# Kernel tuning notes

Measured on AMD Instinct MI355X. Metric: run time of the kernel, lower is better.

## Reference

```python
import jax, jax.numpy as jnp
import numpy as np

B, C, H, W = 32, 384, 32, 32
NH = 4            # num_heads
CC = 192          # conv_channels = ceil(384/2)
HID = 1536        # mlp hidden = 4*dim
EPS = 1e-6


def _ln2d(x, w, b):
    # LayerNorm over channel axis of NCHW
    u = x.mean(1, keepdims=True)
    s = ((x - u) ** 2).mean(1, keepdims=True)
    return w[:, None, None] * ((x - u) * jax.lax.rsqrt(s + EPS)) + b[:, None, None]


def setup_inputs() -> dict:
    key = jax.random.key(0)
    ks = jax.random.split(key, 8)
    f = lambda k, shp, sc: jax.random.normal(k, shp, jnp.float32) * sc
    return {
        "x": f(ks[0], (B, C, H, W), 1.0),
        "conv_w": f(ks[1], (CC, 1, 3, 3), 0.1),
        "conv_b": jnp.zeros((CC,), jnp.float32),
        "nxca_w": jnp.ones((C,), jnp.float32),
        "nxca_b": jnp.zeros((C,), jnp.float32),
        "temp": jnp.ones((NH, 1, 1), jnp.float32),
        "qkv_w": f(ks[2], (3 * C, C), 0.05),
        "qkv_b": jnp.zeros((3 * C,), jnp.float32),
        "proj_w": f(ks[3], (C, C), 0.05),
        "proj_b": jnp.zeros((C,), jnp.float32),
        "norm_w": jnp.ones((C,), jnp.float32),
        "norm_b": jnp.zeros((C,), jnp.float32),
        "fc1_w": f(ks[4], (HID, C), 0.05),
        "fc1_b": jnp.zeros((HID,), jnp.float32),
        "fc2_w": f(ks[5], (C, HID), 0.05),
        "fc2_b": jnp.zeros((C,), jnp.float32),
        "gamma_xca": jnp.ones((C,), jnp.float32),
        "gamma": jnp.ones((C,), jnp.float32),
    }


def reference(x, conv_w, conv_b, nxca_w, nxca_b, temp, qkv_w, qkv_b,
              proj_w, proj_b, norm_w, norm_b, fc1_w, fc1_b, fc2_w, fc2_b,
              gamma_xca, gamma):
    b, c, h, w = x.shape
    n = h * w
    hd = c // NH
    # depthwise 3x3 conv on first CC channels (in-place in torch -> shortcut
    # taken AFTER the conv, faithfully reproduced here)
    xc = jax.lax.conv_general_dilated(
        x[:, :CC], conv_w, (1, 1), ((1, 1), (1, 1)), feature_group_count=CC
    ) + conv_b[None, :, None, None]
    x = jnp.concatenate([xc, x[:, CC:]], axis=1)
    shortcut = x
    # XCA branch
    y = _ln2d(x, nxca_w, nxca_b)
    yf = y.reshape(b, c, n).transpose(0, 2, 1)                       # [B,N,C]
    qkv = (yf @ qkv_w.T + qkv_b).reshape(b, n, 3, NH, hd).transpose(2, 0, 3, 1, 4)
    q, k, v = qkv[0], qkv[1], qkv[2]                                  # [B,h,N,hd]
    q = q / jnp.maximum(jnp.linalg.norm(q, axis=-1, keepdims=True), 1e-12)
    k = k / jnp.maximum(jnp.linalg.norm(k, axis=-1, keepdims=True), 1e-12)
    attn = jax.nn.softmax(jnp.einsum('bhnd,bhmd->bhnm', q, k) * temp, axis=-1)
    o = jnp.einsum('bhnm,bhmd->bhnd', attn, v).transpose(0, 2, 1, 3).reshape(b, n, c)
    o = (o @ proj_w.T + proj_b).transpose(0, 2, 1).reshape(b, c, h, w)
    x = shortcut + gamma_xca[None, :, None, None] * o
    # MLP branch
    shortcut2 = x
    z = _ln2d(x, norm_w, norm_b).transpose(0, 2, 3, 1).reshape(b, n, c)
    z = jax.nn.gelu(z @ fc1_w.T + fc1_b, approximate=False) @ fc2_w.T + fc2_b
    z = z.reshape(b, h, w, c).transpose(0, 3, 1, 2)
    return shortcut2 + gamma[None, :, None, None] * z
```

## Files before the change

### kernel.cpp

```cpp
#include <hip/hip_runtime.h>
#include <cstdint>

typedef unsigned short u16;
typedef unsigned int u32;
typedef unsigned long long u64;
typedef __attribute__((ext_vector_type(4))) float f32x4;
typedef __attribute__((ext_vector_type(8))) __bf16 bf16x8;
typedef __attribute__((ext_vector_type(8))) u16 u16x8;

#define DEV __device__ __forceinline__

DEV u16 cvt16(float f) {
  __bf16 h = (__bf16)f;
  return __builtin_bit_cast(u16, h);
}
DEV u16 f2bf(float f) {
  u32 u = __builtin_bit_cast(u32, f);
  u += 0x7fffu + ((u >> 16) & 1u);
  return (u16)(u >> 16);
}
DEV float bflo2f(u32 packed) { return __builtin_bit_cast(float, packed << 16); }
DEV float bfhi2f(u32 packed) { return __builtin_bit_cast(float, packed & 0xffff0000u); }

DEV void g2l16(void* lds_wave_base, const void* gsrc) {
  __builtin_amdgcn_global_load_lds(
      (const __attribute__((address_space(1))) u32*)gsrc,
      (__attribute__((address_space(3))) u32*)lds_wave_base, 16, 0, 0);
}

DEV float gelu_tanh(float v) {
  float z = v * (0.7978845608f + 0.0356774081f * v * v);
  float e = __expf(2.0f * z);
  float th = 1.0f - 2.0f / (e + 1.0f);
  return 0.5f * v * (1.0f + th);
}

__global__ __launch_bounds__(256) void conv_k(const float* __restrict__ x,
                                              const float* __restrict__ cw,
                                              const float* __restrict__ cb,
                                              float* __restrict__ xc) {
  const int bc = blockIdx.x;
  const int c = bc % 384;
  const int p4 = threadIdx.x * 4;
  const float* xp = x + ((size_t)bc << 10);
  float* op = xc + ((size_t)bc << 10) + p4;
  if (c >= 192) {
    *(f32x4*)op = *(const f32x4*)(xp + p4);
    return;
  }
  const int hh = p4 >> 5, ww0 = p4 & 31;
  const float* wb = cw + c * 9;
  float b0 = cb[c];
  float a0 = b0, a1 = b0, a2 = b0, a3 = b0;
#pragma unroll
  for (int dy = 0; dy < 3; ++dy) {
    int y = hh + dy - 1;
    if ((unsigned)y < 32u) {
      const float* rp = xp + y * 32 + ww0;
      f32x4 m = *(const f32x4*)rp;
      float lft = (ww0 > 0) ? rp[-1] : 0.f;
      float rgt = (ww0 < 28) ? rp[4] : 0.f;
      float w0 = wb[dy * 3], w1 = wb[dy * 3 + 1], w2 = wb[dy * 3 + 2];
      a0 += lft * w0 + m[0] * w1 + m[1] * w2;
      a1 += m[0] * w0 + m[1] * w1 + m[2] * w2;
      a2 += m[1] * w0 + m[2] * w1 + m[3] * w2;
      a3 += m[2] * w0 + m[3] * w1 + rgt * w2;
    }
  }
  f32x4 r = {a0, a1, a2, a3};
  *(f32x4*)op = r;
}

__global__ __launch_bounds__(256) void cvt4_k(const float* __restrict__ s0,
                                              const float* __restrict__ s1,
                                              const float* __restrict__ s2,
                                              const float* __restrict__ s3,
                                              u16* __restrict__ d0,
                                              u16* __restrict__ d1,
                                              u16* __restrict__ d2,
                                              u16* __restrict__ d3) {
  int id = blockIdx.x * 256 + threadIdx.x;
  if (id < 442368) d0[id] = f2bf(s0[id]);
  else if (id < 589824) d1[id - 442368] = f2bf(s1[id - 442368]);
  else if (id < 1179648) d2[id - 589824] = f2bf(s2[id - 589824]);
  else if (id < 1769472) d3[id - 1179648] = f2bf(s3[id - 1179648]);
}

__global__ __launch_bounds__(256) void ln_t_k(const float* __restrict__ X,
                                              const float* __restrict__ w,
                                              const float* __restrict__ bsh,
                                              u16* __restrict__ Y) {
  __shared__ float tile[384][33];
  __shared__ float ps[8][32], ps2[8][32];
  __shared__ float mean_s[32], rstd_s[32];
  const int b = blockIdx.y;
  const int p0 = blockIdx.x * 32;
  const int t = threadIdx.x;
  const int pl = t & 31, cg = t >> 5;
  const float* xb = X + (((size_t)b * 384) << 10) + p0 + pl;
  float s = 0.f, s2 = 0.f;
  for (int c = cg; c < 384; c += 8) {
    float v = xb[(size_t)c << 10];
    tile[c][pl] = v;
    s += v;
    s2 += v * v;
  }
  ps[cg][pl] = s;
  ps2[cg][pl] = s2;
  __syncthreads();
  if (t < 32) {
    float a = 0.f, a2 = 0.f;
#pragma unroll
    for (int g = 0; g < 8; ++g) { a += ps[g][t]; a2 += ps2[g][t]; }
    float mu = a * (1.f / 384.f);
    float var = a2 * (1.f / 384.f) - mu * mu;
    mean_s[t] = mu;
    rstd_s[t] = rsqrtf(var + 1e-6f);
  }
  __syncthreads();
  const int cl = t & 63, pg = t >> 6;
  for (int p = pg; p < 32; p += 4) {
    float mu = mean_s[p], rs = rstd_s[p];
    size_t orow = (((size_t)b << 10) + p0 + p) * 384;
#pragma unroll
    for (int cc = 0; cc < 6; ++cc) {
      int c = cc * 64 + cl;
      float v = (tile[c][p] - mu) * rs * w[c] + bsh[c];
      Y[orow + c] = f2bf(v);
    }
  }
}

__global__ __launch_bounds__(256) void normqk_k(u16* __restrict__ QKV,
                                                const float* __restrict__ temp) {
  const int t = threadIdx.x;
  const int w = t >> 6, l = t & 63;
  const int rg = l >> 4, li = l & 15;
  const int tok = blockIdx.x * 16 + w * 4 + rg;
  u16* rowp = QKV + (size_t)tok * 1152;
#pragma unroll
  for (int seg = 0; seg < 8; ++seg) {
    const int h = seg & 3, isK = seg >> 2;
    u16* p = rowp + isK * 384 + h * 96 + li * 6;
    u32 a = *(const u32*)p;
    u32 b2 = *(const u32*)(p + 2);
    u32 c = *(const u32*)(p + 4);
    float v[6] = {bflo2f(a), bfhi2f(a), bflo2f(b2), bfhi2f(b2), bflo2f(c), bfhi2f(c)};
    float ss = 0.f;
#pragma unroll
    for (int i = 0; i < 6; ++i) ss += v[i] * v[i];
#pragma unroll
    for (int mk = 1; mk < 16; mk <<= 1) ss += __shfl_xor(ss, mk, 64);
    float sc = 1.0f / fmaxf(sqrtf(ss), 1e-12f);
    if (!isK) sc *= temp[h];
    u32 o0 = (u32)f2bf(v[0] * sc) | ((u32)f2bf(v[1] * sc) << 16);
    u32 o1 = (u32)f2bf(v[2] * sc) | ((u32)f2bf(v[3] * sc) << 16);
    u32 o2 = (u32)f2bf(v[4] * sc) | ((u32)f2bf(v[5] * sc) << 16);
    *(u32*)p = o0;
    *(u32*)(p + 2) = o1;
    *(u32*)(p + 4) = o2;
  }
}

__global__ __launch_bounds__(256) void attn_k(const u16* __restrict__ QKV,
                                              const u16* __restrict__ Vg,
                                              u16* __restrict__ O,
                                              const float* __restrict__ temp) {
  __shared__ u16 Kt[2][8192];
  __shared__ u16 Vt[2][6144];
  __shared__ u16 Pt[4][2304];
  const int t = threadIdx.x;
  const int w = t >> 6, l = t & 63;
  const int l15 = l & 15, kg = l >> 4;
  const int id = blockIdx.x;
  const int xcd = id & 7, jj = id >> 3;
  const int bh = xcd * 16 + (jj >> 3);
  const int qb = jj & 7;
  const int b = bh >> 2, h = bh & 3;
  const int q0 = qb * 128 + w * 32;
  const u16* Qb = QKV + (size_t)b * 1024 * 1152;
  const char* Kbg = (const char*)QKV + (size_t)b * 1024 * 2304 + 768 + 192 * h;
  const u16* Vbg = Vg + (size_t)bh * 98304;
  const float T = fabsf(temp[h]);

  u32 sK[4], sV[3];
#pragma unroll
  for (int j = 0; j < 4; ++j) {
    u32 s = w * 4096 + j * 1024 + l * 16;
    u32 row = s >> 8, rem = s & 255;
    u32 X = rem ^ ((row & 7) << 4);
    sK[j] = (X < 192) ? (row * 2304 + X) : 0u;
  }
#pragma unroll
  for (int j = 0; j < 3; ++j) {
    u32 s = w * 3072 + j * 1024 + l * 16;
    u32 u = s ^ (((s >> 7) & 7) << 4);
    sV[j] = (u >> 7) * 2048 + (u & 127);
  }
  u32 cs[3];
#pragma unroll
  for (int kk = 0; kk < 3; ++kk)
    cs[kk] = (u32)((kk * 64 + kg * 16) ^ ((l15 & 7) << 4));

  bf16x8 qf[2][3];
#pragma unroll
  for (int f = 0; f < 2; ++f) {
    const u16* qp = Qb + (size_t)(q0 + f * 16 + l15) * 1152 + h * 96 + kg * 8;
#pragma unroll
    for (int kk = 0; kk < 3; ++kk) qf[f][kk] = *(const bf16x8*)(qp + kk * 32);
  }
  f32x4 oa[2][6];
#pragma unroll
  for (int f = 0; f < 2; ++f)
#pragma unroll
    for (int d = 0; d < 6; ++d) oa[f][d] = {0.f, 0.f, 0.f, 0.f};
  float l_r[2][4] = {{0.f, 0.f, 0.f, 0.f}, {0.f, 0.f, 0.f, 0.f}};
  __bf16* Pw = (__bf16*)&Pt[w][0];

#define STAGE(buf, kv0)                                                        \
  {                                                                            \
    const char* kb = Kbg + (size_t)(kv0) * 2304;                               \
    const char* vb = (const char*)Vbg + (size_t)(kv0) * 2;                     \
    char* kd = (char*)&Kt[buf][0] + w * 4096;                                  \
    char* vd = (char*)&Vt[buf][0] + w * 3072;                                  \
    g2l16(kd, kb + sK[0]);                                                     \
    g2l16(kd + 1024, kb + sK[1]);                                              \
    g2l16(kd + 2048, kb + sK[2]);                                              \
    g2l16(kd + 3072, kb + sK[3]);                                              \
    g2l16(vd, vb + sV[0]);                                                     \
    g2l16(vd + 1024, vb + sV[1]);                                              \
    g2l16(vd + 2048, vb + sV[2]);                                              \
  }

  STAGE(0, 0);
  for (int tt = 0; tt < 16; ++tt) {
    const int cur = tt & 1;
    if (tt < 15) {
      STAGE(cur ^ 1, (tt + 1) * 64);
      asm volatile("s_waitcnt vmcnt(7)" ::: "memory");
    } else {
      asm volatile("s_waitcnt vmcnt(0)" ::: "memory");
    }
    __builtin_amdgcn_s_barrier();
    const char* Kc = (const char*)&Kt[cur][0];
    const char* Vc = (const char*)&Vt[cur][0];
    f32x4 s0[4], s1[4];
#pragma unroll
    for (int n = 0; n < 4; ++n) { s0[n] = {0.f, 0.f, 0.f, 0.f}; s1[n] = {0.f, 0.f, 0.f, 0.f}; }
#pragma unroll
    for (int n = 0; n < 4; ++n) {
      const char* krow = Kc + ((n * 16 + l15) << 8);
#pragma unroll
      for (int kk = 0; kk < 3; ++kk) {
        bf16x8 kf = *(const bf16x8*)(krow + cs[kk]);
        s0[n] = __builtin_amdgcn_mfma_f32_16x16x32_bf16(qf[0][kk], kf, s0[n], 0, 0, 0);
        s1[n] = __builtin_amdgcn_mfma_f32_16x16x32_bf16(qf[1][kk], kf, s1[n], 0, 0, 0);
      }
    }
#pragma unroll
    for (int n = 0; n < 4; ++n) {
#pragma unroll
      for (int j = 0; j < 4; ++j) {
        float p0 = __expf(s0[n][j] - T);
        float p1 = __expf(s1[n][j] - T);
        l_r[0][j] += p0;
        l_r[1][j] += p1;
        Pw[(kg * 4 + j) * 72 + n * 16 + l15] = (__bf16)p0;
        Pw[(16 + kg * 4 + j) * 72 + n * 16 + l15] = (__bf16)p1;
      }
    }
#pragma unroll
    for (int kk = 0; kk < 2; ++kk) {
      bf16x8 pf0 = *(const bf16x8*)(Pw + (size_t)l15 * 72 + kk * 32 + kg * 8);
      bf16x8 pf1 = *(const bf16x8*)(Pw + (size_t)(16 + l15) * 72 + kk * 32 + kg * 8);
#pragma unroll
      for (int d = 0; d < 6; ++d) {
        bf16x8 vf = *(const bf16x8*)(Vc + ((d * 16 + l15) << 7) + cs[kk]);
        oa[0][d] = __builtin_amdgcn_mfma_f32_16x16x32_bf16(pf0, vf, oa[0][d], 0, 0, 0);
        oa[1][d] = __builtin_amdgcn_mfma_f32_16x16x32_bf16(pf1, vf, oa[1][d], 0, 0, 0);
      }
    }
    __builtin_amdgcn_s_barrier();
  }
#undef STAGE
  float inv[2][4];
#pragma unroll
  for (int f = 0; f < 2; ++f)
#pragma unroll
    for (int j = 0; j < 4; ++j) {
      float sum = l_r[f][j];
#pragma unroll
      for (int mk = 1; mk < 16; mk <<= 1) sum += __shfl_xor(sum, mk, 64);
      inv[f][j] = 1.0f / sum;
    }
#pragma unroll
  for (int f = 0; f < 2; ++f)
#pragma unroll
    for (int d = 0; d < 6; ++d)
#pragma unroll
      for (int j = 0; j < 4; ++j) {
        int tok = q0 + f * 16 + kg * 4 + j;
        O[((size_t)b * 1024 + tok) * 384 + h * 96 + d * 16 + l15] =
            f2bf(oa[f][d][j] * inv[f][j]);
      }
}

template <int EPI, int SWZ>
__global__ __launch_bounds__(256) void gemm_k(const u16* __restrict__ A,
                                              const u16* __restrict__ B, int M,
                                              int N, int K,
                                              const float* __restrict__ bias,
                                              const float* gamma,
                                              const float* res, void* outp,
                                              int nbx) {
  __shared__ u16 SM[16384];
  const int t = threadIdx.x;
  const int w = t >> 6, l = t & 63;
  const int l15 = l & 15, kg = l >> 4;
  int bx, by;
  if (SWZ == 1) {
    int id = blockIdx.x;
    int xcd = id & 7, jj = id >> 3;
    int q = jj / nbx;
    bx = jj - q * nbx;
    by = xcd * 32 + q;
  } else if (SWZ == 2) {
    int id = blockIdx.x;
    int xcd = id & 7, jj = id >> 3;
    by = jj % 3;
    bx = (jj / 3) * 8 + xcd;
  } else {
    bx = blockIdx.x; by = blockIdx.y;
  }
  const int m0 = by * 128, n0 = bx * 128;
  const int wr = w >> 1, wc = w & 1;

  const int off1 = w * 1024 + l * 16;
  const int off2 = 4096 + w * 1024 + l * 16;
  const int r1 = off1 >> 6, c1 = off1 & 63;
  const int r2 = off2 >> 6, c2 = off2 & 63;
  const size_t ldab = (size_t)K * 2;
  const char* pa1 = (const char*)A + (size_t)(m0 + r1) * ldab + c1;
  const char* pa2 = (const char*)A + (size_t)(m0 + r2) * ldab + c2;
  const char* pb1 = (const char*)B + (size_t)(n0 + r1) * ldab + c1;
  const char* pb2 = (const char*)B + (size_t)(n0 + r2) * ldab + c2;
  char* SMc = (char*)SM;

  f32x4 acc[4][4];
#pragma unroll
  for (int m = 0; m < 4; ++m)
#pragma unroll
    for (int n = 0; n < 4; ++n) acc[m][n] = {0.f, 0.f, 0.f, 0.f};

  const int nkt = K >> 5;
  {
    char* ad = SMc + w * 1024;
    char* bd = SMc + 16384 + w * 1024;
    g2l16(ad, pa1); g2l16(ad + 4096, pa2);
    g2l16(bd, pb1); g2l16(bd + 4096, pb2);
  }
  for (int kt = 0; kt < nkt; ++kt) {
    const int buf = kt & 1;
    if (kt + 1 < nkt) {
      const size_t o = (size_t)(kt + 1) * 64;
      char* ad = SMc + (buf ^ 1) * 8192 + w * 1024;
      char* bd = SMc + 16384 + (buf ^ 1) * 8192 + w * 1024;
      g2l16(ad, pa1 + o); g2l16(ad + 4096, pa2 + o);
      g2l16(bd, pb1 + o); g2l16(bd + 4096, pb2 + o);
      asm volatile("s_waitcnt vmcnt(4)" ::: "memory");
    } else {
      asm volatile("s_waitcnt vmcnt(0)" ::: "memory");
    }
    __builtin_amdgcn_s_barrier();
    __builtin_amdgcn_sched_barrier(0);
    const u16* Ab = SM + buf * 4096;
    const u16* Bb = SM + 8192 + buf * 4096;
    bf16x8 af[4], bfr[4];
#pragma unroll
    for (int m = 0; m < 4; ++m)
      af[m] = *(const bf16x8*)(Ab + (wr * 64 + m * 16 + l15) * 32 + kg * 8);
#pragma unroll
    for (int n = 0; n < 4; ++n)
      bfr[n] = *(const bf16x8*)(Bb + (wc * 64 + n * 16 + l15) * 32 + kg * 8);
#pragma unroll
    for (int m = 0; m < 4; ++m)
#pragma unroll
      for (int n = 0; n < 4; ++n)
        acc[m][n] = __builtin_amdgcn_mfma_f32_16x16x32_bf16(af[m], bfr[n], acc[m][n], 0, 0, 0);
    __builtin_amdgcn_sched_barrier(0);
    __builtin_amdgcn_s_barrier();
  }

  if (EPI == 2) {
    float* out = (float*)outp;
#pragma unroll
    for (int m = 0; m < 4; ++m) {
#pragma unroll
      for (int n = 0; n < 4; ++n) {
        int tok = n0 + wc * 64 + n * 16 + l15;
        int bb = tok >> 10, p = tok & 1023;
#pragma unroll
        for (int j = 0; j < 4; ++j) {
          int c = m0 + wr * 64 + m * 16 + kg * 4 + j;
          size_t addr = (((size_t)(bb * 384 + c)) << 10) + p;
          out[addr] = res[addr] + gamma[c] * (acc[m][n][j] + bias[c]);
        }
      }
    }
    return;
  }

  const int sec = (EPI == 4) ? (n0 / 384) : 0;
  if (EPI == 4 && sec == 2) {
    u16* Vp = (u16*)(uintptr_t)gamma;
#pragma unroll
    for (int m = 0; m < 4; ++m) {
      const int tokbase = m0 + wr * 64 + m * 16 + kg * 4;
      const int bb = tokbase >> 10, nb = tokbase & 1023;
#pragma unroll
      for (int n = 0; n < 4; ++n) {
        int within = n0 - 768 + wc * 64 + n * 16 + l15;
        int hh = within / 96;
        int dd = within - hh * 96;
        float bs = bias[768 + within];
        int bh = bb * 4 + hh;
        u64 pk = 0;
#pragma unroll
        for (int j = 0; j < 4; ++j)
          pk |= (u64)cvt16(acc[m][n][j] + bs) << (16 * j);
        *(u64*)(Vp + ((size_t)bh * 96 + dd) * 1024 + nb) = pk;
      }
    }
    return;
  }

  {
    u16* Ct = SM;
    float bs[4];
#pragma unroll
    for (int n = 0; n < 4; ++n) bs[n] = bias[n0 + wc * 64 + n * 16 + l15];
    u16* cw_ = Ct + (wr * 64 + kg * 4) * 128 + wc * 64 + l15;
#pragma unroll
    for (int m = 0; m < 4; ++m)
#pragma unroll
      for (int n = 0; n < 4; ++n)
#pragma unroll
        for (int j = 0; j < 4; ++j) {
          float v = acc[m][n][j] + bs[n];
          if (EPI == 1) v = gelu_tanh(v);
          cw_[(m * 16 + j) * 128 + n * 16] = cvt16(v);
        }
    __syncthreads();
    const int row_l = w * 4 + (l >> 4);
    const int colc = (l & 15) * 8;
    const u16* src = Ct + row_l * 128 + colc;
    if (EPI == 1) {
      u16* dst = (u16*)outp + (size_t)(m0 + row_l) * N + n0 + colc;
#pragma unroll
      for (int rr = 0; rr < 8; ++rr)
        *(u16x8*)(dst + (size_t)rr * 16 * N) =
            *(const u16x8*)(src + rr * 16 * 128);
    } else {
      u16* dst = (u16*)outp + (size_t)(m0 + row_l) * 1152 + n0 + colc;
#pragma unroll
      for (int rr = 0; rr < 8; ++rr)
        *(u16x8*)(dst + (size_t)rr * 16 * 1152) =
            *(const u16x8*)(src + rr * 16 * 128);
    }
  }
}

extern "C" void kernel_launch(void* const* d_in, const int* in_sizes, int n_in,
                              void* d_out, int out_size, void* d_ws,
                              size_t ws_size, hipStream_t stream) {
  const float* x      = (const float*)d_in[0];
  const float* conv_w = (const float*)d_in[1];
  const float* conv_b = (const float*)d_in[2];
  const float* nxca_w = (const float*)d_in[3];
  const float* nxca_b = (const float*)d_in[4];
  const float* temp   = (const float*)d_in[5];
  const float* qkv_w  = (const float*)d_in[6];
  const float* qkv_b  = (const float*)d_in[7];
  const float* proj_w = (const float*)d_in[8];
  const float* proj_b = (const float*)d_in[9];
  const float* norm_w = (const float*)d_in[10];
  const float* norm_b = (const float*)d_in[11];
  const float* fc1_w  = (const float*)d_in[12];
  const float* fc1_b  = (const float*)d_in[13];
  const float* fc2_w  = (const float*)d_in[14];
  const float* fc2_b  = (const float*)d_in[15];
  const float* g_xca  = (const float*)d_in[16];
  const float* g_mlp  = (const float*)d_in[17];
  (void)in_sizes; (void)n_in; (void)out_size; (void)ws_size;

  char* ws = (char*)d_ws;
  float* xc  = (float*)(ws);
  u16* Y     = (u16*)(ws + 50331648);
  u16* QKVr  = (u16*)(ws + 75497472);
  u16* Vt    = (u16*)(ws + 150994944);
  u16* Obuf  = Y;
  u16* H1    = QKVr;
  u16* wq    = (u16*)(ws + 176160768);
  u16* wp    = (u16*)(ws + 177045504);
  u16* w1    = (u16*)(ws + 177340416);
  u16* w2    = (u16*)(ws + 178520064);

  cvt4_k<<<6912, 256, 0, stream>>>(qkv_w, proj_w, fc1_w, fc2_w, wq, wp, w1, w2);

  conv_k<<<12288, 256, 0, stream>>>(x, conv_w, conv_b, xc);
  ln_t_k<<<dim3(32, 32), 256, 0, stream>>>(xc, nxca_w, nxca_b, Y);
  gemm_k<4, 1><<<2304, 256, 0, stream>>>(Y, wq, 32768, 1152, 384, qkv_b,
                                         (const float*)Vt, nullptr, QKVr, 9);
  normqk_k<<<2048, 256, 0, stream>>>(QKVr, temp);
  attn_k<<<1024, 256, 0, stream>>>(QKVr, Vt, Obuf, temp);
  gemm_k<2, 2><<<768, 256, 0, stream>>>(wp, Obuf, 384, 32768, 384,
                                        proj_b, g_xca, xc, xc, 0);
  ln_t_k<<<dim3(32, 32), 256, 0, stream>>>(xc, norm_w, norm_b, Y);
  gemm_k<1, 1><<<3072, 256, 0, stream>>>(Y, w1, 32768, 1536, 384, fc1_b,
                                         nullptr, nullptr, H1, 12);
  gemm_k<2, 2><<<768, 256, 0, stream>>>(w2, H1, 384, 32768, 1536,
                                        fc2_b, g_mlp, xc, (float*)d_out, 0);
}
```

Before: 413.2 us.

## Use 256-row GEMM tiles, fold Q norm into attention, add MFMA priority hints

Adds a 512-thread GEMM kernel with 256x128 tiles for the QKV and FC1 projections to raise data reuse per block. Q normalisation and temperature scaling now happen inside the attention kernel from the register-held Q fragments, folded into an exp2 argument, so the separate pass only normalises K. Also inserts s_setprio around MFMA sections in the attention and GEMM loops and simplifies the remaining gemm_k to the transposed fp32-output epilogue. Risks include lower occupancy from larger tiles and a rounding difference, since Q is now scaled in fp32 after bf16 storage rather than rounded after scaling.

New measurement: 411.6 us. No clear change (-0.4%).

```diff
diff --git a/kernel.cpp b/kernel.cpp
--- a/kernel.cpp
+++ b/kernel.cpp
@@ -131,17 +131,15 @@
   }
 }
 
-__global__ __launch_bounds__(256) void normqk_k(u16* __restrict__ QKV,
-                                                const float* __restrict__ temp) {
+__global__ __launch_bounds__(256) void normk_k(u16* __restrict__ QKV) {
   const int t = threadIdx.x;
   const int w = t >> 6, l = t & 63;
   const int rg = l >> 4, li = l & 15;
   const int tok = blockIdx.x * 16 + w * 4 + rg;
-  u16* rowp = QKV + (size_t)tok * 1152;
-#pragma unroll
-  for (int seg = 0; seg < 8; ++seg) {
-    const int h = seg & 3, isK = seg >> 2;
-    u16* p = rowp + isK * 384 + h * 96 + li * 6;
+  u16* rowp = QKV + (size_t)tok * 1152 + 384;
+#pragma unroll
+  for (int h = 0; h < 4; ++h) {
+    u16* p = rowp + h * 96 + li * 6;
     u32 a = *(const u32*)p;
     u32 b2 = *(const u32*)(p + 2);
     u32 c = *(const u32*)(p + 4);
@@ -152,7 +150,6 @@
 #pragma unroll
     for (int mk = 1; mk < 16; mk <<= 1) ss += __shfl_xor(ss, mk, 64);
     float sc = 1.0f / fmaxf(sqrtf(ss), 1e-12f);
-    if (!isK) sc *= temp[h];
     u32 o0 = (u32)f2bf(v[0] * sc) | ((u32)f2bf(v[1] * sc) << 16);
     u32 o1 = (u32)f2bf(v[2] * sc) | ((u32)f2bf(v[3] * sc) << 16);
     u32 o2 = (u32)f2bf(v[4] * sc) | ((u32)f2bf(v[5] * sc) << 16);
@@ -181,7 +178,8 @@
   const u16* Qb = QKV + (size_t)b * 1024 * 1152;
   const char* Kbg = (const char*)QKV + (size_t)b * 1024 * 2304 + 768 + 192 * h;
   const u16* Vbg = Vg + (size_t)bh * 98304;
-  const float T = fabsf(temp[h]);
+  const float tl2e = temp[h] * 1.44269504f;
+  const float mT2 = -fabsf(temp[h]) * 1.44269504f;
 
   u32 sK[4], sV[3];
 #pragma unroll
@@ -208,6 +206,29 @@
     const u16* qp = Qb + (size_t)(q0 + f * 16 + l15) * 1152 + h * 96 + kg * 8;
 #pragma unroll
     for (int kk = 0; kk < 3; ++kk) qf[f][kk] = *(const bf16x8*)(qp + kk * 32);
+  }
+  float a0[4], a1[4];
+  {
+    float alpha[2];
+#pragma unroll
+    for (int f = 0; f < 2; ++f) {
+      float ss = 0.f;
+#pragma unroll
+      for (int kk = 0; kk < 3; ++kk)
+#pragma unroll
+        for (int e = 0; e < 8; ++e) {
+          float v = (float)qf[f][kk][e];
+          ss += v * v;
+        }
+      ss += __shfl_xor(ss, 16, 64);
+      ss += __shfl_xor(ss, 32, 64);
+      alpha[f] = tl2e * rsqrtf(fmaxf(ss, 1e-24f));
+    }
+#pragma unroll
+    for (int j = 0; j < 4; ++j) {
+      a0[j] = __shfl(alpha[0], kg * 4 + j, 64);
+      a1[j] = __shfl(alpha[1], kg * 4 + j, 64);
+    }
   }
   f32x4 oa[2][6];
 #pragma unroll
@@ -247,6 +268,7 @@
     f32x4 s0[4], s1[4];
 #pragma unroll
     for (int n = 0; n < 4; ++n) { s0[n] = {0.f, 0.f, 0.f, 0.f}; s1[n] = {0.f, 0.f, 0.f, 0.f}; }
+    __builtin_amdgcn_s_setprio(1);
 #pragma unroll
     for (int n = 0; n < 4; ++n) {
       const char* krow = Kc + ((n * 16 + l15) << 8);
@@ -257,18 +279,20 @@
         s1[n] = __builtin_amdgcn_mfma_f32_16x16x32_bf16(qf[1][kk], kf, s1[n], 0, 0, 0);
       }
     }
+    __builtin_amdgcn_s_setprio(0);
 #pragma unroll
     for (int n = 0; n < 4; ++n) {
 #pragma unroll
       for (int j = 0; j < 4; ++j) {
-        float p0 = __expf(s0[n][j] - T);
-        float p1 = __expf(s1[n][j] - T);
+        float p0 = exp2f(fmaf(s0[n][j], a0[j], mT2));
+        float p1 = exp2f(fmaf(s1[n][j], a1[j], mT2));
         l_r[0][j] += p0;
         l_r[1][j] += p1;
         Pw[(kg * 4 + j) * 72 + n * 16 + l15] = (__bf16)p0;
         Pw[(16 + kg * 4 + j) * 72 + n * 16 + l15] = (__bf16)p1;
       }
     }
+    __builtin_amdgcn_s_setprio(1);
 #pragma unroll
     for (int kk = 0; kk < 2; ++kk) {
       bf16x8 pf0 = *(const bf16x8*)(Pw + (size_t)l15 * 72 + kk * 32 + kg * 8);
@@ -280,6 +304,7 @@
         oa[1][d] = __builtin_amdgcn_mfma_f32_16x16x32_bf16(pf1, vf, oa[1][d], 0, 0, 0);
       }
     }
+    __builtin_amdgcn_s_setprio(0);
     __builtin_amdgcn_s_barrier();
   }
 #undef STAGE
@@ -305,45 +330,151 @@
       }
 }
 
-template <int EPI, int SWZ>
+template <int EPI>
+__global__ __launch_bounds__(512) void gemm256_k(const u16* __restrict__ A,
+                                                 const u16* __restrict__ B,
+                                                 int N, int K,
+                                                 const float* __restrict__ bias,
+                                                 u16* __restrict__ vtp,
+                                                 u16* __restrict__ outp,
+                                                 int nbx) {
+  __shared__ u16 SM[24576];
+  const int t = threadIdx.x;
+  const int w = t >> 6, l = t & 63;
+  const int l15 = l & 15, kg = l >> 4;
+  const int id = blockIdx.x;
+  const int xcd = id & 7, jj = id >> 3;
+  const int qq = jj / nbx;
+  const int bx = jj - qq * nbx;
+  const int by = xcd * 16 + qq;
+  const int m0 = by * 256, n0 = bx * 128;
+  const int wr = w >> 1, wc = w & 1;
+  const size_t ldab = (size_t)K * 2;
+  const char* pa1 = (const char*)A + (size_t)(m0 + (t >> 2)) * ldab + (t & 3) * 16;
+  const char* pa2 = pa1 + (size_t)128 * ldab;
+  const char* pb1 = (const char*)B + (size_t)(n0 + (t >> 2)) * ldab + (t & 3) * 16;
+  char* SMc = (char*)SM;
+
+  f32x4 acc[4][4];
+#pragma unroll
+  for (int m = 0; m < 4; ++m)
+#pragma unroll
+    for (int n = 0; n < 4; ++n) acc[m][n] = {0.f, 0.f, 0.f, 0.f};
+
+  const int nkt = K >> 5;
+  g2l16(SMc + w * 1024, pa1);
+  g2l16(SMc + 8192 + w * 1024, pa2);
+  g2l16(SMc + 32768 + w * 1024, pb1);
+  for (int kt = 0; kt < nkt; ++kt) {
+    const int buf = kt & 1;
+    if (kt + 1 < nkt) {
+      const size_t o = (size_t)(kt + 1) * 64;
+      g2l16(SMc + (buf ^ 1) * 16384 + w * 1024, pa1 + o);
+      g2l16(SMc + (buf ^ 1) * 16384 + 8192 + w * 1024, pa2 + o);
+      g2l16(SMc + 32768 + (buf ^ 1) * 8192 + w * 1024, pb1 + o);
+      asm volatile("s_waitcnt vmcnt(3)" ::: "memory");
+    } else {
+      asm volatile("s_waitcnt vmcnt(0)" ::: "memory");
+    }
+    __builtin_amdgcn_s_barrier();
+    __builtin_amdgcn_sched_barrier(0);
+    const u16* Ab = SM + buf * 8192;
+    const u16* Bb = SM + 16384 + buf * 4096;
+    bf16x8 af[4], bfr[4];
+#pragma unroll
+    for (int m = 0; m < 4; ++m)
+      af[m] = *(const bf16x8*)(Ab + (wr * 64 + m * 16 + l15) * 32 + kg * 8);
+#pragma unroll
+    for (int n = 0; n < 4; ++n)
+      bfr[n] = *(const bf16x8*)(Bb + (wc * 64 + n * 16 + l15) * 32 + kg * 8);
+    __builtin_amdgcn_s_setprio(1);
+#pragma unroll
+    for (int m = 0; m < 4; ++m)
+#pragma unroll
+      for (int n = 0; n < 4; ++n)
+        acc[m][n] = __builtin_amdgcn_mfma_f32_16x16x32_bf16(af[m], bfr[n], acc[m][n], 0, 0, 0);
+    __builtin_amdgcn_s_setprio(0);
+    __builtin_amdgcn_sched_barrier(0);
+    __builtin_amdgcn_s_barrier();
+  }
+
+  if (EPI == 4 && n0 >= 768) {
+#pragma unroll
+    for (int m = 0; m < 4; ++m) {
+      const int tokbase = m0 + wr * 64 + m * 16 + kg * 4;
+      const int bb = tokbase >> 10, nb = tokbase & 1023;
+#pragma unroll
+      for (int n = 0; n < 4; ++n) {
+        int within = n0 - 768 + wc * 64 + n * 16 + l15;
+        int hh = within / 96;
+        int dd = within - hh * 96;
+        float bs = bias[768 + within];
+        int bh = bb * 4 + hh;
+        u64 pk = 0;
+#pragma unroll
+        for (int j = 0; j < 4; ++j)
+          pk |= (u64)cvt16(acc[m][n][j] + bs) << (16 * j);
+        *(u64*)(vtp + ((size_t)bh * 96 + dd) * 1024 + nb) = pk;
+      }
+    }
+    return;
+  }
+
+  u16* Ct = SM;
+  float bs[4];
+#pragma unroll
+  for (int n = 0; n < 4; ++n) bs[n] = bias[n0 + wc * 64 + n * 16 + l15];
+  const size_t ostride = (EPI == 4) ? 1152 : (size_t)N;
+#pragma unroll
+  for (int p = 0; p < 2; ++p) {
+    if ((wr >> 1) == p) {
+      u16* cw_ = Ct + ((wr & 1) * 64 + kg * 4) * 128 + wc * 64 + l15;
+#pragma unroll
+      for (int m = 0; m < 4; ++m)
+#pragma unroll
+        for (int n = 0; n < 4; ++n)
+#pragma unroll
+          for (int j = 0; j < 4; ++j) {
+            float v = acc[m][n][j] + bs[n];
+            if (EPI == 1) v = gelu_tanh(v);
+            cw_[(m * 16 + j) * 128 + n * 16] = cvt16(v);
+          }
+    }
+    __syncthreads();
+    const int row_l = t >> 2;
+    const int colc = (t & 3) * 32;
+    const u16* src = Ct + row_l * 128 + colc;
+    u16* dst = outp + (size_t)(m0 + p * 128 + row_l) * ostride + n0 + colc;
+#pragma unroll
+    for (int c4 = 0; c4 < 4; ++c4)
+      *(u16x8*)(dst + c4 * 8) = *(const u16x8*)(src + c4 * 8);
+    __syncthreads();
+  }
+}
+
 __global__ __launch_bounds__(256) void gemm_k(const u16* __restrict__ A,
-                                              const u16* __restrict__ B, int M,
-                                              int N, int K,
+                                              const u16* __restrict__ B,
+                                              int K,
                                               const float* __restrict__ bias,
-                                              const float* gamma,
-                                              const float* res, void* outp,
-                                              int nbx) {
+                                              const float* __restrict__ gamma,
+                                              const float* __restrict__ res,
+                                              float* __restrict__ outp) {
   __shared__ u16 SM[16384];
   const int t = threadIdx.x;
   const int w = t >> 6, l = t & 63;
   const int l15 = l & 15, kg = l >> 4;
-  int bx, by;
-  if (SWZ == 1) {
-    int id = blockIdx.x;
-    int xcd = id & 7, jj = id >> 3;
-    int q = jj / nbx;
-    bx = jj - q * nbx;
-    by = xcd * 32 + q;
-  } else if (SWZ == 2) {
-    int id = blockIdx.x;
-    int xcd = id & 7, jj = id >> 3;
-    by = jj % 3;
-    bx = (jj / 3) * 8 + xcd;
-  } else {
-    bx = blockIdx.x; by = blockIdx.y;
-  }
+  int id = blockIdx.x;
+  int xcd = id & 7, jj = id >> 3;
+  int by = jj % 3;
+  int bx = (jj / 3) * 8 + xcd;
   const int m0 = by * 128, n0 = bx * 128;
   const int wr = w >> 1, wc = w & 1;
 
-  const int off1 = w * 1024 + l * 16;
-  const int off2 = 4096 + w * 1024 + l * 16;
-  const int r1 = off1 >> 6, c1 = off1 & 63;
-  const int r2 = off2 >> 6, c2 = off2 & 63;
   const size_t ldab = (size_t)K * 2;
-  const char* pa1 = (const char*)A + (size_t)(m0 + r1) * ldab + c1;
-  const char* pa2 = (const char*)A + (size_t)(m0 + r2) * ldab + c2;
-  const char* pb1 = (const char*)B + (size_t)(n0 + r1) * ldab + c1;
-  const char* pb2 = (const char*)B + (size_t)(n0 + r2) * ldab + c2;
+  const char* pa1 = (const char*)A + (size_t)(m0 + (t >> 2)) * ldab + (t & 3) * 16;
+  const char* pa2 = pa1 + (size_t)64 * ldab;
+  const char* pb1 = (const char*)B + (size_t)(n0 + (t >> 2)) * ldab + (t & 3) * 16;
+  const char* pb2 = pb1 + (size_t)64 * ldab;
   char* SMc = (char*)SM;
 
   f32x4 acc[4][4];
@@ -382,90 +513,29 @@
 #pragma unroll
     for (int n = 0; n < 4; ++n)
       bfr[n] = *(const bf16x8*)(Bb + (wc * 64 + n * 16 + l15) * 32 + kg * 8);
+    __builtin_amdgcn_s_setprio(1);
 #pragma unroll
     for (int m = 0; m < 4; ++m)
 #pragma unroll
       for (int n = 0; n < 4; ++n)
         acc[m][n] = __builtin_amdgcn_mfma_f32_16x16x32_bf16(af[m], bfr[n], acc[m][n], 0, 0, 0);
+    __builtin_amdgcn_s_setprio(0);
     __builtin_amdgcn_sched_barrier(0);
     __builtin_amdgcn_s_barrier();
   }
 
-  if (EPI == 2) {
-    float* out = (float*)outp;
-#pragma unroll
-    for (int m = 0; m < 4; ++m) {
-#pragma unroll
-      for (int n = 0; n < 4; ++n) {
-        int tok = n0 + wc * 64 + n * 16 + l15;
-        int bb = tok >> 10, p = tok & 1023;
-#pragma unroll
-        for (int j = 0; j < 4; ++j) {
-          int c = m0 + wr * 64 + m * 16 + kg * 4 + j;
-          size_t addr = (((size_t)(bb * 384 + c)) << 10) + p;
-          out[addr] = res[addr] + gamma[c] * (acc[m][n][j] + bias[c]);
-        }
+#pragma unroll
+  for (int m = 0; m < 4; ++m) {
+#pragma unroll
+    for (int n = 0; n < 4; ++n) {
+      int tok = n0 + wc * 64 + n * 16 + l15;
+      int bb = tok >> 10, p = tok & 1023;
+#pragma unroll
+      for (int j = 0; j < 4; ++j) {
+        int c = m0 + wr * 64 + m * 16 + kg * 4 + j;
+        size_t addr = (((size_t)(bb * 384 + c)) << 10) + p;
+        outp[addr] = res[addr] + gamma[c] * (acc[m][n][j] + bias[c]);
       }
-    }
-    return;
-  }
-
-  const int sec = (EPI == 4) ? (n0 / 384) : 0;
-  if (EPI == 4 && sec == 2) {
-    u16* Vp = (u16*)(uintptr_t)gamma;
-#pragma unroll
-    for (int m = 0; m < 4; ++m) {
-      const int tokbase = m0 + wr * 64 + m * 16 + kg * 4;
-      const int bb = tokbase >> 10, nb = tokbase & 1023;
-#pragma unroll
-      for (int n = 0; n < 4; ++n) {
-        int within = n0 - 768 + wc * 64 + n * 16 + l15;
-        int hh = within / 96;
-        int dd = within - hh * 96;
-        float bs = bias[768 + within];
-        int bh = bb * 4 + hh;
-        u64 pk = 0;
-#pragma unroll
-        for (int j = 0; j < 4; ++j)
-          pk |= (u64)cvt16(acc[m][n][j] + bs) << (16 * j);
-        *(u64*)(Vp + ((size_t)bh * 96 + dd) * 1024 + nb) = pk;
-      }
-    }
-    return;
-  }
-
-  {
-    u16* Ct = SM;
-    float bs[4];
-#pragma unroll
-    for (int n = 0; n < 4; ++n) bs[n] = bias[n0 + wc * 64 + n * 16 + l15];
-    u16* cw_ = Ct + (wr * 64 + kg * 4) * 128 + wc * 64 + l15;
-#pragma unroll
-    for (int m = 0; m < 4; ++m)
-#pragma unroll
-      for (int n = 0; n < 4; ++n)
-#pragma unroll
-        for (int j = 0; j < 4; ++j) {
-          float v = acc[m][n][j] + bs[n];
-          if (EPI == 1) v = gelu_tanh(v);
-          cw_[(m * 16 + j) * 128 + n * 16] = cvt16(v);
-        }
-    __syncthreads();
-    const int row_l = w * 4 + (l >> 4);
-    const int colc = (l & 15) * 8;
-    const u16* src = Ct + row_l * 128 + colc;
-    if (EPI == 1) {
-      u16* dst = (u16*)outp + (size_t)(m0 + row_l) * N + n0 + colc;
-#pragma unroll
-      for (int rr = 0; rr < 8; ++rr)
-        *(u16x8*)(dst + (size_t)rr * 16 * N) =
-            *(const u16x8*)(src + rr * 16 * 128);
-    } else {
-      u16* dst = (u16*)outp + (size_t)(m0 + row_l) * 1152 + n0 + colc;
-#pragma unroll
-      for (int rr = 0; rr < 8; ++rr)
-        *(u16x8*)(dst + (size_t)rr * 16 * 1152) =
-            *(const u16x8*)(src + rr * 16 * 128);
     }
   }
 }
@@ -509,15 +579,11 @@
 
   conv_k<<<12288, 256, 0, stream>>>(x, conv_w, conv_b, xc);
   ln_t_k<<<dim3(32, 32), 256, 0, stream>>>(xc, nxca_w, nxca_b, Y);
-  gemm_k<4, 1><<<2304, 256, 0, stream>>>(Y, wq, 32768, 1152, 384, qkv_b,
-                                         (const float*)Vt, nullptr, QKVr, 9);
-  normqk_k<<<2048, 256, 0, stream>>>(QKVr, temp);
+  gemm256_k<4><<<1152, 512, 0, stream>>>(Y, wq, 1152, 384, qkv_b, Vt, QKVr, 9);
+  normk_k<<<2048, 256, 0, stream>>>(QKVr);
   attn_k<<<1024, 256, 0, stream>>>(QKVr, Vt, Obuf, temp);
-  gemm_k<2, 2><<<768, 256, 0, stream>>>(wp, Obuf, 384, 32768, 384,
-                                        proj_b, g_xca, xc, xc, 0);
+  gemm_k<<<768, 256, 0, stream>>>(wp, Obuf, 384, proj_b, g_xca, xc, xc);
   ln_t_k<<<dim3(32, 32), 256, 0, stream>>>(xc, norm_w, norm_b, Y);
-  gemm_k<1, 1><<<3072, 256, 0, stream>>>(Y, w1, 32768, 1536, 384, fc1_b,
-                                         nullptr, nullptr, H1, 12);
-  gemm_k<2, 2><<<768, 256, 0, stream>>>(w2, H1, 384, 32768, 1536,
-                                        fc2_b, g_mlp, xc, (float*)d_out, 0);
-}
+  gemm256_k<1><<<1536, 512, 0, stream>>>(Y, w1, 1536, 384, fc1_b, nullptr, H1, 12);
+  gemm_k<<<768, 256, 0, stream>>>(w2, H1, 1536, fc2_b, g_mlp, xc, (float*)d_out);
+}
```
